# Kernel optimization log

Hardware: AMD Instinct MI355X
Metric: run time of the kernel (lower is better)

Reference implementation:

```python
import itertools
import jax, jax.numpy as jnp
import numpy as np

DIM = 448
HEADS = 8
KEY_DIM = 32
ATTN_RATIO = 4
RES = 7
N = RES * RES  # 49 tokens
D_V = KEY_DIM * ATTN_RATIO  # 128
DH = D_V * HEADS  # 1024
H_QKV = DH + 2 * KEY_DIM * HEADS  # 1536
HIDDEN = 4 * DIM  # 1792
SCALE = KEY_DIM ** -0.5
LS_INIT = 1e-05
B = 1024


def _build_bias_idx():
    points = list(itertools.product(range(RES), range(RES)))
    offsets = {}
    idxs = []
    for p1 in points:
        for p2 in points:
            off = (abs(p1[0] - p2[0]), abs(p1[1] - p2[1]))
            if off not in offsets:
                offsets[off] = len(offsets)
            idxs.append(offsets[off])
    return np.array(idxs, dtype=np.int32).reshape(N, N), len(offsets)


def setup_inputs() -> dict:
    key = jax.random.key(0)
    ks = jax.random.split(key, 16)
    bias_idx_np, n_off = _build_bias_idx()
    s = lambda fan: 1.0 / np.sqrt(fan)
    return {
        "x": jax.random.normal(ks[0], (B, N, DIM), jnp.float32),
        "qkv_w": jax.random.normal(ks[1], (H_QKV, DIM), jnp.float32) * s(DIM),
        "qkv_b": jnp.zeros((H_QKV,), jnp.float32),
        "proj_w": jax.random.normal(ks[2], (DIM, DH), jnp.float32) * s(DH),
        "proj_b": jnp.zeros((DIM,), jnp.float32),
        "fc1_w": jax.random.normal(ks[3], (HIDDEN, DIM), jnp.float32) * s(DIM),
        "fc1_b": jnp.zeros((HIDDEN,), jnp.float32),
        "fc2_w": jax.random.normal(ks[4], (DIM, HIDDEN), jnp.float32) * s(HIDDEN),
        "fc2_b": jnp.zeros((DIM,), jnp.float32),
        "norm1_g": jnp.ones((DIM,), jnp.float32),
        "norm1_b": jnp.zeros((DIM,), jnp.float32),
        "norm2_g": jnp.ones((DIM,), jnp.float32),
        "norm2_b": jnp.zeros((DIM,), jnp.float32),
        "ls1_gamma": jnp.full((DIM,), LS_INIT, jnp.float32),
        "ls2_gamma": jnp.full((DIM,), LS_INIT, jnp.float32),
        "attn_biases": jax.random.normal(ks[5], (HEADS, n_off), jnp.float32) * 0.02,
        "bias_idx": jnp.asarray(bias_idx_np),
    }


def _ln(x, g, b, eps=1e-5):
    mu = jnp.mean(x, axis=-1, keepdims=True)
    var = jnp.mean(jnp.square(x - mu), axis=-1, keepdims=True)
    return (x - mu) * jax.lax.rsqrt(var + eps) * g + b


def reference(x, qkv_w, qkv_b, proj_w, proj_b, fc1_w, fc1_b, fc2_w, fc2_b,
              norm1_g, norm1_b, norm2_g, norm2_b, ls1_gamma, ls2_gamma,
              attn_biases, bias_idx):
    Bk, Nk, C = x.shape
    # --- token mixer: attention with gathered relative-position bias ---
    h = _ln(x, norm1_g, norm1_b)
    qkv = (h @ qkv_w.T + qkv_b).reshape(Bk, Nk, HEADS, -1)
    q, k, v = jnp.split(qkv, [KEY_DIM, 2 * KEY_DIM], axis=3)
    # scores: [B, H, N, N]
    attn = jnp.einsum('bnhd,bmhd->bhnm', q, k) * SCALE
    attn = attn + attn_biases[:, bias_idx]  # gather bias [H, N, N]
    attn = jax.nn.softmax(attn, axis=-1)
    out = jnp.einsum('bhnm,bmhd->bnhd', attn, v).reshape(Bk, Nk, DH)
    out = out @ proj_w.T + proj_b
    x = x + out * ls1_gamma
    # --- MLP ---
    h2 = _ln(x, norm2_g, norm2_b)
    h2 = jax.nn.gelu(h2 @ fc1_w.T + fc1_b, approximate=False)
    h2 = h2 @ fc2_w.T + fc2_b
    x = x + h2 * ls2_gamma
    return x
```

## Files before the change

### kernel.cpp

```cpp
#include <hip/hip_runtime.h>
#include <hip/hip_bf16.h>
#include <hip/hip_fp8.h>


#define NTOK 49
#define CDIM 448
#define NHEAD 8
#define DHID 1024
#define HQKV 1536
#define FHID 1792
#define QK_SCALE 0.1767766952966369f
#define INV_SCALE 5.656854249492381f

typedef __attribute__((ext_vector_type(8))) short bf16x8;
typedef __attribute__((ext_vector_type(4))) float f32x4;
typedef unsigned int u32;
typedef unsigned char u8;

__device__ __forceinline__ short f2b(float f) {
    __hip_bfloat16 h = __float2bfloat16(f);
    return *reinterpret_cast<short*>(&h);
}
__device__ __forceinline__ u8 f2f8(float f) {
    __hip_fp8_e4m3 h(f);
    return *reinterpret_cast<u8*>(&h);
}

__device__ __forceinline__ u32 pack_off(int row, int k, int nkp) {
    return (u32)(((row >> 4) * nkp + (k >> 5)) << 9) +
           (u32)((((k & 31) >> 3) << 7) + ((row & 15) << 3) + (k & 7));
}

__device__ __forceinline__ void gll16(const void* g, void* l) {
    __builtin_amdgcn_global_load_lds(
        (const __attribute__((address_space(1))) u32*)g,
        (__attribute__((address_space(3))) u32*)l, 16, 0, 0);
}

__global__ __launch_bounds__(256) void convert_w(
    const float* __restrict__ s0, const float* __restrict__ s1,
    const float* __restrict__ s2, const float* __restrict__ s3,
    u8* __restrict__ d0, u8* __restrict__ d1,
    u8* __restrict__ d2, u8* __restrict__ d3,
    const float* __restrict__ biases, const int* __restrict__ bidx,
    float* __restrict__ bfull)
{
    int i = blockIdx.x * 256 + threadIdx.x;
    if (i < 688128) {
        int n = i / 448, k = i - n * 448;
        d0[pack_off(n, k, 14)] = f2f8(s0[i]);
    }
    if (i < 458752) {
        int n = i >> 10, k = i & 1023;
        d1[pack_off(n, k, 32)] = f2f8(s1[i]);
    }
    if (i < 802816) {
        int n2 = i / 448, k2 = i - n2 * 448;
        d2[pack_off(n2, k2, 14)] = f2f8(s2[i]);
        int n3 = i / 1792, k3 = i - n3 * 1792;
        d3[pack_off(n3, k3, 56)] = f2f8(s3[i]);
    }
    if (i < NHEAD * NTOK * NTOK) {
        int h = i / (NTOK * NTOK), p = i % (NTOK * NTOK);
        bfull[i] = biases[h * NTOK + bidx[p]];
    }
}

__global__ __launch_bounds__(256) void ln_kernel(
    const float* __restrict__ x, u8* __restrict__ out,
    const float* __restrict__ g, const float* __restrict__ b)
{
    int row = blockIdx.x * 4 + (threadIdx.x >> 6);
    int lane = threadIdx.x & 63;
    const float* xr = x + (size_t)row * CDIM;
    float v[7];
    float s = 0.f;
#pragma unroll
    for (int i = 0; i < 7; i++) { v[i] = xr[i * 64 + lane]; s += v[i]; }
#pragma unroll
    for (int o = 32; o > 0; o >>= 1) s += __shfl_xor(s, o, 64);
    float mean = s * (1.0f / 448.0f);
    float q = 0.f;
#pragma unroll
    for (int i = 0; i < 7; i++) { float d = v[i] - mean; q += d * d; }
#pragma unroll
    for (int o = 32; o > 0; o >>= 1) q += __shfl_xor(q, o, 64);
    float rstd = rsqrtf(q * (1.0f / 448.0f) + 1e-5f);
#pragma unroll
    for (int i = 0; i < 7; i++) {
        int c = i * 64 + lane;
        out[pack_off(row, c, 14)] = f2f8((v[i] - mean) * rstd * g[c] + b[c]);
    }
}

template <int EPI>
__global__ __launch_bounds__(256, 4) void gemm_bt(
    const u8* __restrict__ A,
    const u8* __restrict__ W,
    const float* __restrict__ bias,
    const float* __restrict__ ls,
    const float* resid,
    float* outF,
    void* outX,
    int M, int N, int K)
{
    __shared__ __align__(16) u8 sA[3][4096];
    __shared__ __align__(16) u8 sB[3][4096];
    const int tid = threadIdx.x;
    const int lane = tid & 63;
    const int w = tid >> 6;
    const int lr = lane & 15, lq = lane >> 4;

    const int gx = gridDim.x;
    const int nwg = gx * gridDim.y;
    const int lin = blockIdx.y * gx + blockIdx.x;
    const int q8 = nwg >> 3, r8 = nwg & 7;
    const int xcd = lin & 7, sub = lin >> 3;
    const int wg = (xcd < r8 ? xcd * (q8 + 1) : r8 * (q8 + 1) + (xcd - r8) * q8) + sub;
    const int m0 = (wg / gx) * 128;
    const int n0 = (wg % gx) * 128;

    const int nkp = K >> 5;
    const int maxpB = (N >> 4) - 1;
    int prA = (m0 >> 4) + 2 * w + (lane >> 5);
    int prB = (n0 >> 4) + 2 * w + (lane >> 5);
    prB = prB < maxpB ? prB : maxpB;
    u32 oA = (u32)(prA * nkp) * 512u + (u32)((lane & 31) * 16);
    u32 oB = (u32)(prB * nkp) * 512u + (u32)((lane & 31) * 16);
    const int dst = w * 1024;

    const f32x4 fz = {0.f, 0.f, 0.f, 0.f};
    f32x4 acc[4][4];
#pragma unroll
    for (int i = 0; i < 4; i++)
#pragma unroll
        for (int j = 0; j < 4; j++) acc[i][j] = fz;

    const int rdA = (w & 1) * 2048 + lq * 128 + lr * 8;
    const int rdB = (w >> 1) * 2048 + lq * 128 + lr * 8;

    const int nt = K >> 5;
    gll16(A + oA, sA[0] + dst); gll16(W + oB, sB[0] + dst); oA += 512; oB += 512;
    gll16(A + oA, sA[1] + dst); gll16(W + oB, sB[1] + dst); oA += 512; oB += 512;

    int bc = 0;
    int bs = 2;
    for (int t = 0; t < nt; t++) {
        if (t + 1 < nt) asm volatile("s_waitcnt vmcnt(2)" ::: "memory");
        else            asm volatile("s_waitcnt vmcnt(0)" ::: "memory");
        __builtin_amdgcn_s_barrier();
        if (t + 2 < nt) {
            gll16(A + oA, sA[bs] + dst);
            gll16(W + oB, sB[bs] + dst);
            oA += 512; oB += 512;
            bs = (bs == 2) ? 0 : bs + 1;
        }
        const u8* baseA = sA[bc] + rdA;
        const u8* baseB = sB[bc] + rdB;
        bc = (bc == 2) ? 0 : bc + 1;
        long af[4], bfr[4];
#pragma unroll
        for (int i = 0; i < 4; i++) af[i] = *(const long*)(baseA + i * 512);
#pragma unroll
        for (int j = 0; j < 4; j++) bfr[j] = *(const long*)(baseB + j * 512);
        __builtin_amdgcn_s_setprio(1);
#pragma unroll
        for (int i = 0; i < 4; i++)
#pragma unroll
            for (int j = 0; j < 4; j++)
                acc[i][j] = __builtin_amdgcn_mfma_f32_16x16x32_fp8_fp8(
                    af[i], bfr[j], acc[i][j], 0, 0, 0);
        __builtin_amdgcn_s_setprio(0);
    }

    const int wm = (w & 1) * 64, wn = (w >> 1) * 64;
#pragma unroll
    for (int i = 0; i < 4; i++)
#pragma unroll
        for (int j = 0; j < 4; j++)
#pragma unroll
            for (int r = 0; r < 4; r++) {
                int row = m0 + wm + i * 16 + lq * 4 + r;
                int col = n0 + wn + j * 16 + lr;
                if (col < N) {
                    float v = acc[i][j][r] + bias[col];
                    if (EPI == 0) {
                        ((short*)outX)[(size_t)row * N + col] = f2b(v);
                    } else if (EPI == 1) {
                        float gl = v / (1.0f + __expf(-1.702f * v));
                        ((u8*)outX)[pack_off(row, col, N >> 5)] = f2f8(gl);
                    } else {
                        outF[(size_t)row * N + col] =
                            resid[(size_t)row * N + col] + v * ls[col];
                    }
                }
            }
}

__global__ __launch_bounds__(64) void attn_mfma(
    const short* __restrict__ qkv,
    const float* __restrict__ bfull,
    u8* __restrict__ attn_out)
{
    __shared__ short sP[64 * 72];
    const int head = blockIdx.x;
    const size_t base = (size_t)blockIdx.y * NTOK;
    const int lane = threadIdx.x;
    const int lr = lane & 15, lq = lane >> 4;

    f32x4 sc[4][4];
#pragma unroll
    for (int i = 0; i < 4; i++)
#pragma unroll
        for (int j = 0; j < 4; j++)
#pragma unroll
            for (int r = 0; r < 4; r++) {
                int row = i * 16 + lq * 4 + r, col = j * 16 + lr;
                float v;
                if (col >= NTOK)      v = -1e30f;
                else if (row < NTOK)  v = bfull[head * (NTOK * NTOK) + row * NTOK + col] * INV_SCALE;
                else                  v = 0.f;
                sc[i][j][r] = v;
            }

    bf16x8 qf[4], kf[4];
#pragma unroll
    for (int i = 0; i < 4; i++) {
        int r = i * 16 + lr; r = r < NTOK ? r : NTOK - 1;
        const short* rp = qkv + (base + r) * HQKV + head * 192;
        qf[i] = *(const bf16x8*)(rp + lq * 8);
        kf[i] = *(const bf16x8*)(rp + 32 + lq * 8);
    }
#pragma unroll
    for (int i = 0; i < 4; i++)
#pragma unroll
        for (int j = 0; j < 4; j++)
            sc[i][j] = __builtin_amdgcn_mfma_f32_16x16x32_bf16(
                qf[i], kf[j], sc[i][j], 0, 0, 0);

#pragma unroll
    for (int i = 0; i < 4; i++)
#pragma unroll
        for (int r = 0; r < 4; r++) {
            float s0 = sc[i][0][r] * QK_SCALE;
            float s1 = sc[i][1][r] * QK_SCALE;
            float s2 = sc[i][2][r] * QK_SCALE;
            float s3 = sc[i][3][r] * QK_SCALE;
            float m = fmaxf(fmaxf(s0, s1), fmaxf(s2, s3));
#pragma unroll
            for (int o = 1; o < 16; o <<= 1) m = fmaxf(m, __shfl_xor(m, o, 64));
            float e0 = __expf(s0 - m), e1 = __expf(s1 - m);
            float e2 = __expf(s2 - m), e3 = __expf(s3 - m);
            float l = e0 + e1 + e2 + e3;
#pragma unroll
            for (int o = 1; o < 16; o <<= 1) l += __shfl_xor(l, o, 64);
            float inv = 1.0f / l;
            short* pr = &sP[(i * 16 + lq * 4 + r) * 72];
            pr[lr]      = f2b(e0 * inv);
            pr[16 + lr] = f2b(e1 * inv);
            pr[32 + lr] = f2b(e2 * inv);
            pr[48 + lr] = f2b(e3 * inv);
        }

    bf16x8 pa[4][2];
#pragma unroll
    for (int i = 0; i < 4; i++)
#pragma unroll
        for (int kk = 0; kk < 2; kk++)
            pa[i][kk] = *(const bf16x8*)&sP[(i * 16 + lr) * 72 + kk * 32 + lq * 8];

#pragma unroll
    for (int half = 0; half < 2; half++) {
        const f32x4 fz = {0.f, 0.f, 0.f, 0.f};
        f32x4 o[4][4];
        bf16x8 pb[4][2];
#pragma unroll
        for (int j = 0; j < 4; j++)
#pragma unroll
            for (int kk = 0; kk < 2; kk++) {
                const int d = half * 64 + j * 16 + lr;
                const short* vcol = qkv + head * 192 + 64 + d;
                bf16x8 tvec;
#pragma unroll
                for (int e = 0; e < 8; e++) {
                    int tok = kk * 32 + lq * 8 + e;
                    tvec[e] = tok < NTOK ? vcol[(base + tok) * HQKV] : (short)0;
                }
                pb[j][kk] = tvec;
            }
#pragma unroll
        for (int i = 0; i < 4; i++)
#pragma unroll
            for (int j = 0; j < 4; j++) {
                o[i][j] = __builtin_amdgcn_mfma_f32_16x16x32_bf16(
                    pa[i][0], pb[j][0], fz, 0, 0, 0);
                o[i][j] = __builtin_amdgcn_mfma_f32_16x16x32_bf16(
                    pa[i][1], pb[j][1], o[i][j], 0, 0, 0);
            }
#pragma unroll
        for (int i = 0; i < 4; i++)
#pragma unroll
            for (int j = 0; j < 4; j++)
#pragma unroll
                for (int r = 0; r < 4; r++) {
                    int row = i * 16 + lq * 4 + r;
                    if (row < NTOK)
                        attn_out[pack_off((int)(base + row),
                                          head * 128 + half * 64 + j * 16 + lr, 32)] =
                            f2f8(o[i][j][r]);
                }
    }
}

extern "C" void kernel_launch(void* const* d_in, const int* in_sizes, int n_in,
                              void* d_out, int out_size, void* d_ws, size_t ws_size,
                              hipStream_t stream) {
    const float* x      = (const float*)d_in[0];
    const float* qkv_w  = (const float*)d_in[1];
    const float* qkv_b  = (const float*)d_in[2];
    const float* proj_w = (const float*)d_in[3];
    const float* proj_b = (const float*)d_in[4];
    const float* fc1_w  = (const float*)d_in[5];
    const float* fc1_b  = (const float*)d_in[6];
    const float* fc2_w  = (const float*)d_in[7];
    const float* fc2_b  = (const float*)d_in[8];
    const float* n1g    = (const float*)d_in[9];
    const float* n1b    = (const float*)d_in[10];
    const float* n2g    = (const float*)d_in[11];
    const float* n2b    = (const float*)d_in[12];
    const float* ls1    = (const float*)d_in[13];
    const float* ls2    = (const float*)d_in[14];
    const float* biases = (const float*)d_in[15];
    const int*   bidx   = (const int*)d_in[16];
    float* outp = (float*)d_out;

    char* ws = (char*)d_ws;
    u8* Wq = (u8*)ws; ws += 688128;
    u8* Wp = (u8*)ws; ws += 458752;
    u8* W1 = (u8*)ws; ws += 802816;
    u8* W2 = (u8*)ws; ws += 802816;
    float* bfull = (float*)ws; ws += (size_t)NHEAD * NTOK * NTOK * 4;
    const size_t fixed = 2752512 + (size_t)NHEAD * NTOK * NTOK * 4;

    int IC = 1024;
    while (IC > 128) {
        size_t Rr = (size_t)IC * NTOK;
        if (fixed + Rr * 4544ull <= ws_size) break;
        IC >>= 1;
    }
    const size_t R = (size_t)IC * NTOK;
    u8*    hbuf = (u8*)ws;    ws += R * CDIM;
    short* qkvb = (short*)ws; ws += R * HQKV * 2;
    u8*    attb = (u8*)ws;    ws += R * DHID;
    u8*    gbuf = (u8*)qkvb;

    convert_w<<<3136, 256, 0, stream>>>(qkv_w, proj_w, fc1_w, fc2_w,
                                        Wq, Wp, W1, W2, biases, bidx, bfull);

    for (int c0 = 0; c0 < 1024; c0 += IC) {
        const float* xc = x + (size_t)c0 * NTOK * CDIM;
        float* oc = outp + (size_t)c0 * NTOK * CDIM;
        const int Ri = IC * NTOK;
        const int gy = (Ri + 127) / 128;

        ln_kernel<<<Ri / 4, 256, 0, stream>>>(xc, hbuf, n1g, n1b);
        gemm_bt<0><<<dim3(HQKV / 128, gy), 256, 0, stream>>>(
            hbuf, Wq, qkv_b, nullptr, nullptr, nullptr, (void*)qkvb, Ri, HQKV, CDIM);
        attn_mfma<<<dim3(NHEAD, IC), 64, 0, stream>>>(qkvb, bfull, attb);
        gemm_bt<2><<<dim3(4, gy), 256, 0, stream>>>(
            attb, Wp, proj_b, ls1, xc, oc, nullptr, Ri, CDIM, DHID);
        ln_kernel<<<Ri / 4, 256, 0, stream>>>(oc, hbuf, n2g, n2b);
        gemm_bt<1><<<dim3(FHID / 128, gy), 256, 0, stream>>>(
            hbuf, W1, fc1_b, nullptr, nullptr, nullptr, (void*)gbuf, Ri, FHID, CDIM);
        gemm_bt<2><<<dim3(4, gy), 256, 0, stream>>>(
            gbuf, W2, fc2_b, ls2, oc, oc, nullptr, Ri, CDIM, FHID);
    }
}
```

Measured before the change: 736.8 us.

## Split attention kernel across four wavefronts, one 16-row query tile each

The attention kernel goes from one 64-lane wavefront per (head, batch) to four wavefronts, each owning a 16-row query tile. This cuts per-thread register use (score and output accumulators drop from 16 tiles to 4) and gives the scheduler more waves to hide latency. In exchange, each wave reloads the K fragments and the full V columns, so global and L2 traffic for K and V rises about fourfold.

After: 722.6 us. About the same (-1.9%).

```diff
diff --git a/kernel.cpp b/kernel.cpp
--- a/kernel.cpp
+++ b/kernel.cpp
@@ -197,82 +197,77 @@
             }
 }
 
-__global__ __launch_bounds__(64) void attn_mfma(
+__global__ __launch_bounds__(256) void attn_mfma(
     const short* __restrict__ qkv,
     const float* __restrict__ bfull,
     u8* __restrict__ attn_out)
 {
-    __shared__ short sP[64 * 72];
+    __shared__ short sP[4][16 * 72];
     const int head = blockIdx.x;
     const size_t base = (size_t)blockIdx.y * NTOK;
-    const int lane = threadIdx.x;
+    const int tid = threadIdx.x;
+    const int lane = tid & 63;
+    const int wi = tid >> 6;
     const int lr = lane & 15, lq = lane >> 4;
 
-    f32x4 sc[4][4];
-#pragma unroll
-    for (int i = 0; i < 4; i++)
-#pragma unroll
-        for (int j = 0; j < 4; j++)
-#pragma unroll
-            for (int r = 0; r < 4; r++) {
-                int row = i * 16 + lq * 4 + r, col = j * 16 + lr;
-                float v;
-                if (col >= NTOK)      v = -1e30f;
-                else if (row < NTOK)  v = bfull[head * (NTOK * NTOK) + row * NTOK + col] * INV_SCALE;
-                else                  v = 0.f;
-                sc[i][j][r] = v;
-            }
-
-    bf16x8 qf[4], kf[4];
-#pragma unroll
-    for (int i = 0; i < 4; i++) {
-        int r = i * 16 + lr; r = r < NTOK ? r : NTOK - 1;
-        const short* rp = qkv + (base + r) * HQKV + head * 192;
-        qf[i] = *(const bf16x8*)(rp + lq * 8);
-        kf[i] = *(const bf16x8*)(rp + 32 + lq * 8);
-    }
-#pragma unroll
-    for (int i = 0; i < 4; i++)
-#pragma unroll
-        for (int j = 0; j < 4; j++)
-            sc[i][j] = __builtin_amdgcn_mfma_f32_16x16x32_bf16(
-                qf[i], kf[j], sc[i][j], 0, 0, 0);
-
-#pragma unroll
-    for (int i = 0; i < 4; i++)
+    f32x4 sc[4];
+#pragma unroll
+    for (int j = 0; j < 4; j++)
 #pragma unroll
         for (int r = 0; r < 4; r++) {
-            float s0 = sc[i][0][r] * QK_SCALE;
-            float s1 = sc[i][1][r] * QK_SCALE;
-            float s2 = sc[i][2][r] * QK_SCALE;
-            float s3 = sc[i][3][r] * QK_SCALE;
-            float m = fmaxf(fmaxf(s0, s1), fmaxf(s2, s3));
-#pragma unroll
-            for (int o = 1; o < 16; o <<= 1) m = fmaxf(m, __shfl_xor(m, o, 64));
-            float e0 = __expf(s0 - m), e1 = __expf(s1 - m);
-            float e2 = __expf(s2 - m), e3 = __expf(s3 - m);
-            float l = e0 + e1 + e2 + e3;
-#pragma unroll
-            for (int o = 1; o < 16; o <<= 1) l += __shfl_xor(l, o, 64);
-            float inv = 1.0f / l;
-            short* pr = &sP[(i * 16 + lq * 4 + r) * 72];
-            pr[lr]      = f2b(e0 * inv);
-            pr[16 + lr] = f2b(e1 * inv);
-            pr[32 + lr] = f2b(e2 * inv);
-            pr[48 + lr] = f2b(e3 * inv);
+            int row = wi * 16 + lq * 4 + r, col = j * 16 + lr;
+            float v;
+            if (col >= NTOK)      v = -1e30f;
+            else if (row < NTOK)  v = bfull[head * (NTOK * NTOK) + row * NTOK + col] * INV_SCALE;
+            else                  v = 0.f;
+            sc[j][r] = v;
         }
 
-    bf16x8 pa[4][2];
-#pragma unroll
-    for (int i = 0; i < 4; i++)
-#pragma unroll
-        for (int kk = 0; kk < 2; kk++)
-            pa[i][kk] = *(const bf16x8*)&sP[(i * 16 + lr) * 72 + kk * 32 + lq * 8];
+    bf16x8 qf, kf[4];
+    {
+        int r = wi * 16 + lr; r = r < NTOK ? r : NTOK - 1;
+        qf = *(const bf16x8*)(qkv + (base + r) * HQKV + head * 192 + lq * 8);
+    }
+#pragma unroll
+    for (int j = 0; j < 4; j++) {
+        int r = j * 16 + lr; r = r < NTOK ? r : NTOK - 1;
+        kf[j] = *(const bf16x8*)(qkv + (base + r) * HQKV + head * 192 + 32 + lq * 8);
+    }
+#pragma unroll
+    for (int j = 0; j < 4; j++)
+        sc[j] = __builtin_amdgcn_mfma_f32_16x16x32_bf16(qf, kf[j], sc[j], 0, 0, 0);
+
+#pragma unroll
+    for (int r = 0; r < 4; r++) {
+        float s0 = sc[0][r] * QK_SCALE;
+        float s1 = sc[1][r] * QK_SCALE;
+        float s2 = sc[2][r] * QK_SCALE;
+        float s3 = sc[3][r] * QK_SCALE;
+        float m = fmaxf(fmaxf(s0, s1), fmaxf(s2, s3));
+#pragma unroll
+        for (int o = 1; o < 16; o <<= 1) m = fmaxf(m, __shfl_xor(m, o, 64));
+        float e0 = __expf(s0 - m), e1 = __expf(s1 - m);
+        float e2 = __expf(s2 - m), e3 = __expf(s3 - m);
+        float l = e0 + e1 + e2 + e3;
+#pragma unroll
+        for (int o = 1; o < 16; o <<= 1) l += __shfl_xor(l, o, 64);
+        float inv = 1.0f / l;
+        short* pr = &sP[wi][(lq * 4 + r) * 72];
+        pr[lr]      = f2b(e0 * inv);
+        pr[16 + lr] = f2b(e1 * inv);
+        pr[32 + lr] = f2b(e2 * inv);
+        pr[48 + lr] = f2b(e3 * inv);
+    }
+
+    bf16x8 pa[2];
+#pragma unroll
+    for (int kk = 0; kk < 2; kk++)
+        pa[kk] = *(const bf16x8*)&sP[wi][lr * 72 + kk * 32 + lq * 8];
 
 #pragma unroll
     for (int half = 0; half < 2; half++) {
         const f32x4 fz = {0.f, 0.f, 0.f, 0.f};
-        f32x4 o[4][4];
+        f32x4 o[4];
         bf16x8 pb[4][2];
 #pragma unroll
         for (int j = 0; j < 4; j++)
@@ -289,26 +284,20 @@
                 pb[j][kk] = tvec;
             }
 #pragma unroll
-        for (int i = 0; i < 4; i++)
-#pragma unroll
-            for (int j = 0; j < 4; j++) {
-                o[i][j] = __builtin_amdgcn_mfma_f32_16x16x32_bf16(
-                    pa[i][0], pb[j][0], fz, 0, 0, 0);
-                o[i][j] = __builtin_amdgcn_mfma_f32_16x16x32_bf16(
-                    pa[i][1], pb[j][1], o[i][j], 0, 0, 0);
+        for (int j = 0; j < 4; j++) {
+            o[j] = __builtin_amdgcn_mfma_f32_16x16x32_bf16(pa[0], pb[j][0], fz, 0, 0, 0);
+            o[j] = __builtin_amdgcn_mfma_f32_16x16x32_bf16(pa[1], pb[j][1], o[j], 0, 0, 0);
+        }
+#pragma unroll
+        for (int j = 0; j < 4; j++)
+#pragma unroll
+            for (int r = 0; r < 4; r++) {
+                int row = wi * 16 + lq * 4 + r;
+                if (row < NTOK)
+                    attn_out[pack_off((int)(base + row),
+                                      head * 128 + half * 64 + j * 16 + lr, 32)] =
+                        f2f8(o[j][r]);
             }
-#pragma unroll
-        for (int i = 0; i < 4; i++)
-#pragma unroll
-            for (int j = 0; j < 4; j++)
-#pragma unroll
-                for (int r = 0; r < 4; r++) {
-                    int row = i * 16 + lq * 4 + r;
-                    if (row < NTOK)
-                        attn_out[pack_off((int)(base + row),
-                                          head * 128 + half * 64 + j * 16 + lr, 32)] =
-                            f2f8(o[i][j][r]);
-                }
     }
 }
 
@@ -366,7 +355,7 @@
         ln_kernel<<<Ri / 4, 256, 0, stream>>>(xc, hbuf, n1g, n1b);
         gemm_bt<0><<<dim3(HQKV / 128, gy), 256, 0, stream>>>(
             hbuf, Wq, qkv_b, nullptr, nullptr, nullptr, (void*)qkvb, Ri, HQKV, CDIM);
-        attn_mfma<<<dim3(NHEAD, IC), 64, 0, stream>>>(qkvb, bfull, attb);
+        attn_mfma<<<dim3(NHEAD, IC), 256, 0, stream>>>(qkvb, bfull, attb);
         gemm_bt<2><<<dim3(4, gy), 256, 0, stream>>>(
             attb, Wp, proj_b, ls1, xc, oc, nullptr, Ri, CDIM, DHID);
         ln_kernel<<<Ri / 4, 256, 0, stream>>>(oc, hbuf, n2g, n2b);
```
